# Kernel optimization log

Measured on AMD Instinct MI355X. Metric: run time of the kernel, lower is better.

## Reference

```python
import jax, jax.numpy as jnp
import numpy as np

N, E, DIN, EIN, H, R, G, DEPTH = 50000, 800000, 64, 16, 300, 1024, 256, 5


def setup_inputs() -> dict:
    key = jax.random.key(0)
    ks = jax.random.split(key, 16)
    x = jax.random.normal(ks[0], (N, DIN), jnp.float32)
    edge_attr = jax.random.normal(ks[1], (E, EIN), jnp.float32)
    edge_index = jax.random.randint(ks[2], (2, E), 0, N, dtype=jnp.int32)
    batch = jnp.sort(jax.random.randint(ks[3], (N,), 0, G, dtype=jnp.int32))
    def lin(k, fan_in, shape):
        return jax.random.normal(k, shape, jnp.float32) / np.sqrt(fan_in)
    return {
        "x": x,
        "edge_attr": edge_attr,
        "edge_index": edge_index,
        "batch": batch,
        "W_pn": lin(ks[4], DIN, (DIN, H)),
        "b_pn": jnp.zeros((H,), jnp.float32),
        "W_pe": lin(ks[5], EIN, (EIN, H)),
        "b_pe": jnp.zeros((H,), jnp.float32),
        "W1": lin(ks[6], H, (DEPTH, H, H)),
        "b1": jnp.zeros((DEPTH, H), jnp.float32),
        "W2": lin(ks[7], H, (DEPTH, H, H)),
        "b2": jnp.zeros((DEPTH, H), jnp.float32),
        "W_sp": lin(ks[8], H, (H, R)),
        "b_sp": jnp.zeros((R,), jnp.float32),
        "prelu_a": jnp.float32(0.25),
    }


def reference(x, edge_attr, edge_index, batch, W_pn, b_pn, W_pe, b_pe,
              W1, b1, W2, b2, W_sp, b_sp, prelu_a):
    src = edge_index[0]  # message source (x_j)
    dst = edge_index[1]  # aggregation target
    # input projections
    h = jax.nn.relu(x @ W_pn + b_pn)          # [N, H]
    e = edge_attr @ W_pe + b_pe               # [E, H]
    for i in range(DEPTH):
        # GINEConv: sum_j ReLU(x_j + e_ji), eps = 0
        m = jax.nn.relu(h[src] + e)            # [E, H]
        agg = jax.ops.segment_sum(m, dst, num_segments=N)  # [N, H]
        z = h + agg
        z = jax.nn.relu(z @ W1[i] + b1[i]) @ W2[i] + b2[i]
        h = jax.nn.relu(z) if i < DEPTH - 1 else z
        # dropout is identity in eval mode
    pooled = jax.ops.segment_sum(h, batch, num_segments=G)  # [G, H]
    out = pooled @ W_sp + b_sp                 # [G, R]
    # PReLU with a single learned slope
    return jnp.where(out >= 0, out, prelu_a * out)
```

## Files before the change

### kernel.cpp

```cpp
#include <hip/hip_runtime.h>
#include <hip/hip_bf16.h>

#define N_NODES 50000
#define N_EDGES 800000
#define DIN_    64
#define EIN_    16
#define H_      300
#define R_OUT   1024
#define G_GR    256
#define DEPTH_  5
#define KPAD    320
#define NPAD    50048
#define ESLOT   20

typedef unsigned short ushort_t;
typedef __attribute__((ext_vector_type(8))) short bf16x8;
typedef __attribute__((ext_vector_type(4))) short s16x4;
typedef __attribute__((ext_vector_type(4))) float f32x4;

__device__ __forceinline__ ushort_t f2b(float f) {
  unsigned x = __float_as_uint(f);
  unsigned r = (x + 0x7fffu + ((x >> 16) & 1u)) >> 16;
  return (ushort_t)r;
}
__device__ __forceinline__ float b2f(ushort_t u) {
  return __uint_as_float((unsigned)u << 16);
}

__global__ void pack_weights(const float* __restrict__ W1, const float* __restrict__ W2,
                             ushort_t* __restrict__ Bp1, ushort_t* __restrict__ Bp2) {
  int idx = blockIdx.x * 256 + threadIdx.x;
  const int per = DEPTH_ * 40 * KPAD * 8;
  if (idx >= 2 * per) return;
  const float* W = W1;
  ushort_t* Bp = Bp1;
  int t = idx;
  if (t >= per) { t -= per; W = W2; Bp = Bp2; }
  int j  = t & 7;
  int n  = (t >> 3) % KPAD;
  int kg = ((t >> 3) / KPAD) % 40;
  int i  = t / (40 * KPAD * 8);
  int k  = kg * 8 + j;
  float v = (k < H_ && n < H_) ? W[(i * H_ + k) * H_ + n] : 0.f;
  Bp[t] = f2b(v);
}

__global__ void pack_wpe(const float* __restrict__ Wpe, const float* __restrict__ bpe,
                         ushort_t* __restrict__ Bpe) {
  int t = blockIdx.x * 256 + threadIdx.x;
  if (t >= 4 * KPAD * 8) return;
  int j  = t & 7;
  int n  = (t >> 3) % KPAD;
  int kg = (t >> 3) / KPAD;
  int k  = kg * 8 + j;
  float v = 0.f;
  if (n < H_) {
    if (k < EIN_) v = Wpe[k * H_ + n];
    else if (k == EIN_) v = bpe[n];
  }
  Bpe[t] = f2b(v);
}

__global__ void pack_wpn(const float* __restrict__ Wpn, ushort_t* __restrict__ Bpn) {
  int t = blockIdx.x * 256 + threadIdx.x;
  if (t >= 8 * KPAD * 8) return;
  int j  = t & 7;
  int n  = (t >> 3) % KPAD;
  int kg = (t >> 3) / KPAD;
  int k  = kg * 8 + j;
  float v = (n < H_) ? Wpn[k * H_ + n] : 0.f;
  Bpn[t] = f2b(v);
}

__global__ void hist_deg(const int* __restrict__ dst, int* __restrict__ deg) {
  int e = blockIdx.x * 256 + threadIdx.x;
  if (e < N_EDGES) atomicAdd(deg + dst[e], 1);
}

__global__ __launch_bounds__(1024) void exscan_kernel(const int* __restrict__ deg,
                                                      int* __restrict__ off) {
  __shared__ int wsum[16];
  __shared__ int carry_s;
  int lane = threadIdx.x & 63;
  int wv = threadIdx.x >> 6;
  if (threadIdx.x == 0) carry_s = 0;
  __syncthreads();
  for (int base = 0; base < N_NODES; base += 1024) {
    int i = base + (int)threadIdx.x;
    int orig = (i < N_NODES) ? deg[i] : 0;
    int v = orig;
#pragma unroll
    for (int s = 1; s < 64; s <<= 1) {
      int u = __shfl_up(v, s);
      if (lane >= s) v += u;
    }
    if (lane == 63) wsum[wv] = v;
    __syncthreads();
    if (wv == 0) {
      int t = (lane < 16) ? wsum[lane] : 0;
#pragma unroll
      for (int s = 1; s < 16; s <<= 1) {
        int u = __shfl_up(t, s);
        if (lane >= s) t += u;
      }
      if (lane < 16) wsum[lane] = t;
    }
    __syncthreads();
    int wbase = (wv > 0) ? wsum[wv - 1] : 0;
    if (i < N_NODES) off[i] = carry_s + wbase + v - orig;
    __syncthreads();
    if (threadIdx.x == 1023) carry_s += wsum[15];
    __syncthreads();
  }
  if (threadIdx.x == 0) off[N_NODES] = carry_s;
}

__global__ void scatter_edges(const int* __restrict__ src, const int* __restrict__ dst,
                              int* __restrict__ cursor, int* __restrict__ csr_src,
                              int* __restrict__ csr_eid) {
  int e = blockIdx.x * 256 + threadIdx.x;
  if (e >= N_EDGES) return;
  int d = dst[e];
  int pos = atomicAdd(cursor + d, 1);
  csr_src[pos] = src[e];
  csr_eid[pos] = e;
}

__global__ __launch_bounds__(256) void proj_gemm(const float* __restrict__ x,
                                                 const ushort_t* __restrict__ Bpn,
                                                 const float* __restrict__ bpn,
                                                 ushort_t* __restrict__ hb) {
  int lane = threadIdx.x & 63;
  int wid  = threadIdx.x >> 6;
  int lr = lane & 15, lg = lane >> 4;
  int rowblk  = blockIdx.x * 64 + (wid & 1) * 32;
  int colbase = (wid >> 1) * 160;
  int ar0 = rowblk + lr;       if (ar0 >= N_NODES) ar0 = 0;
  int ar1 = rowblk + 16 + lr;  if (ar1 >= N_NODES) ar1 = 0;
  f32x4 acc[2][10];
#pragma unroll
  for (int a = 0; a < 2; ++a)
#pragma unroll
    for (int c = 0; c < 10; ++c) acc[a][c] = (f32x4){0.f, 0.f, 0.f, 0.f};

#pragma unroll
  for (int ks = 0; ks < 2; ++ks) {
    int k0 = ks * 32;
    const float* xr0 = x + (size_t)ar0 * DIN_ + k0 + lg * 8;
    const float* xr1 = x + (size_t)ar1 * DIN_ + k0 + lg * 8;
    f32x4 l0 = *(const f32x4*)xr0, h0 = *(const f32x4*)(xr0 + 4);
    f32x4 l1 = *(const f32x4*)xr1, h1 = *(const f32x4*)(xr1 + 4);
    bf16x8 a0, a1;
#pragma unroll
    for (int j = 0; j < 4; ++j) {
      a0[j] = (short)f2b(l0[j]); a0[j + 4] = (short)f2b(h0[j]);
      a1[j] = (short)f2b(l1[j]); a1[j + 4] = (short)f2b(h1[j]);
    }
    const ushort_t* bb = Bpn + ((unsigned)(k0 / 8 + lg) * KPAD + colbase + lr) * 8;
#pragma unroll
    for (int c = 0; c < 10; ++c) {
      bf16x8 b = *(const bf16x8*)(bb + c * 16 * 8);
      acc[0][c] = __builtin_amdgcn_mfma_f32_16x16x32_bf16(a0, b, acc[0][c], 0, 0, 0);
      acc[1][c] = __builtin_amdgcn_mfma_f32_16x16x32_bf16(a1, b, acc[1][c], 0, 0, 0);
    }
  }
#pragma unroll
  for (int rt = 0; rt < 2; ++rt) {
#pragma unroll
    for (int c = 0; c < 10; ++c) {
      int col = colbase + c * 16 + lr;
      float bv = (col < H_) ? bpn[col] : 0.f;
#pragma unroll
      for (int r = 0; r < 4; ++r) {
        int row = rowblk + rt * 16 + lg * 4 + r;
        if (row >= N_NODES) continue;
        float v = fmaxf(acc[rt][c][r] + bv, 0.f);
        if (col >= H_) v = 0.f;
        hb[(unsigned)row * KPAD + col] = f2b(v);
      }
    }
  }
}

__global__ __launch_bounds__(320) void node_agg_mfma(const ushort_t* __restrict__ hb,
                                                     const float* __restrict__ ea,
                                                     const ushort_t* __restrict__ Bpe,
                                                     const int* __restrict__ csr_src,
                                                     const int* __restrict__ csr_eid,
                                                     const int* __restrict__ off,
                                                     ushort_t* zb) {
  __shared__ ushort_t lds_e[2 * KPAD * ESLOT];
  int n = blockIdx.x;
  int tid = threadIdx.x;
  if (n >= N_NODES) {
    zb[(unsigned)n * KPAD + tid] = 0;
    return;
  }
  int lane = tid & 63;
  int w = tid >> 6;
  int lr = lane & 15, lg = lane >> 4;
  int p0 = __builtin_amdgcn_readfirstlane(off[n]);
  int p1 = __builtin_amdgcn_readfirstlane(off[n + 1]);
  unsigned zi = (unsigned)n * KPAD + tid;
  float self = b2f(hb[zi]);

  bf16x8 bfr[4];
#pragma unroll
  for (int t = 0; t < 4; ++t) {
    int col = w * 64 + t * 16 + lr;
    bfr[t] = *(const bf16x8*)(Bpe + ((unsigned)lg * KPAD + col) * 8);
  }

  float acc = 0.f;
  int ci = 0;
  for (int pc = p0; pc < p1; pc += 16, ci ^= 1) {
    int eid = csr_eid[pc + lr];
    bf16x8 afr = (bf16x8){0, 0, 0, 0, 0, 0, 0, 0};
    if (lg < 2) {
      const float* ar = ea + (size_t)eid * EIN_ + lg * 8;
      f32x4 lo = *(const f32x4*)ar;
      f32x4 hi = *(const f32x4*)(ar + 4);
#pragma unroll
      for (int j = 0; j < 4; ++j) {
        afr[j] = (short)f2b(lo[j]);
        afr[j + 4] = (short)f2b(hi[j]);
      }
    } else if (lg == 2) {
      afr[0] = (short)0x3F80;
    }
    int ebase = lg * 4;
    ushort_t* ldsb = lds_e + ci * (KPAD * ESLOT);
#pragma unroll
    for (int t = 0; t < 4; ++t) {
      f32x4 e4 = __builtin_amdgcn_mfma_f32_16x16x32_bf16(afr, bfr[t], (f32x4){0.f, 0.f, 0.f, 0.f}, 0, 0, 0);
      int col = w * 64 + t * 16 + lr;
      s16x4 pk;
#pragma unroll
      for (int r = 0; r < 4; ++r)
        pk[r] = (short)((pc + ebase + r < p1) ? f2b(e4[r]) : (ushort_t)0xFF80);
      *(s16x4*)(ldsb + (unsigned)col * ESLOT + ebase) = pk;
    }
    int sv = csr_src[pc + lr];
    __syncthreads();
    const ushort_t* ldsr = lds_e + ci * (KPAD * ESLOT) + (unsigned)tid * ESLOT;
#pragma unroll
    for (int eq = 0; eq < 4; ++eq) {
      if (pc + eq * 4 >= p1) break;
      s16x4 ep = *(const s16x4*)(ldsr + eq * 4);
#pragma unroll
      for (int r = 0; r < 4; ++r) {
        int s = __builtin_amdgcn_readlane(sv, eq * 4 + r);
        float g = b2f(hb[(unsigned)s * KPAD + tid]);
        acc += fmaxf(g + b2f((ushort_t)ep[r]), 0.f);
      }
    }
  }
  zb[zi] = f2b(self + acc);
}

template <int RELU_OUT, int OUT_BF16>
__global__ __launch_bounds__(256) void gemm300(const ushort_t* A,
                                               const ushort_t* __restrict__ Bp,
                                               const float* __restrict__ bias,
                                               void* Cout) {
  int lane = threadIdx.x & 63;
  int wid  = threadIdx.x >> 6;
  int lr = lane & 15, lg = lane >> 4;
  int rowblk  = blockIdx.x * 128 + (wid & 1) * 64;
  int colbase = (wid >> 1) * 160;
  f32x4 acc[4][10];
#pragma unroll
  for (int a = 0; a < 4; ++a)
#pragma unroll
    for (int c = 0; c < 10; ++c) acc[a][c] = (f32x4){0.f, 0.f, 0.f, 0.f};

  const ushort_t* Ap = A + (unsigned)(rowblk + lr) * KPAD + lg * 8;
  for (int k0 = 0; k0 < KPAD; k0 += 32) {
    bf16x8 a0 = *(const bf16x8*)(Ap + k0);
    bf16x8 a1 = *(const bf16x8*)(Ap + 16 * KPAD + k0);
    bf16x8 a2 = *(const bf16x8*)(Ap + 32 * KPAD + k0);
    bf16x8 a3 = *(const bf16x8*)(Ap + 48 * KPAD + k0);
    const ushort_t* bb = Bp + ((unsigned)(k0 / 8 + lg) * KPAD + colbase + lr) * 8;
#pragma unroll
    for (int c = 0; c < 10; ++c) {
      bf16x8 b = *(const bf16x8*)(bb + c * 16 * 8);
      acc[0][c] = __builtin_amdgcn_mfma_f32_16x16x32_bf16(a0, b, acc[0][c], 0, 0, 0);
      acc[1][c] = __builtin_amdgcn_mfma_f32_16x16x32_bf16(a1, b, acc[1][c], 0, 0, 0);
      acc[2][c] = __builtin_amdgcn_mfma_f32_16x16x32_bf16(a2, b, acc[2][c], 0, 0, 0);
      acc[3][c] = __builtin_amdgcn_mfma_f32_16x16x32_bf16(a3, b, acc[3][c], 0, 0, 0);
    }
  }
  __syncthreads();
#pragma unroll
  for (int rt = 0; rt < 4; ++rt) {
#pragma unroll
    for (int c = 0; c < 10; ++c) {
      int col = colbase + c * 16 + lr;
      float bv = (col < H_) ? bias[col] : 0.f;
#pragma unroll
      for (int r = 0; r < 4; ++r) {
        int row = rowblk + rt * 16 + lg * 4 + r;
        if (row >= N_NODES) continue;
        float v = acc[rt][c][r] + bv;
        if (RELU_OUT) v = fmaxf(v, 0.f);
        if (OUT_BF16) {
          ((ushort_t*)Cout)[(unsigned)row * KPAD + col] = f2b(v);
        } else if (col < H_) {
          ((float*)Cout)[(unsigned)row * H_ + col] = v;
        }
      }
    }
  }
}

__global__ void pool_kernel(const float* __restrict__ h, const int* __restrict__ batch,
                            float* __restrict__ pooled) {
  int g = blockIdx.x;
  int hh = threadIdx.x;
  int lo = 0, hi = N_NODES;
  while (lo < hi) { int mid = (lo + hi) >> 1; if (batch[mid] < g) lo = mid + 1; else hi = mid; }
  int start = lo;
  hi = N_NODES;
  while (lo < hi) { int mid = (lo + hi) >> 1; if (batch[mid] < g + 1) lo = mid + 1; else hi = mid; }
  int end = lo;
  if (hh >= H_) return;
  float s = 0.f;
  for (int n = start; n < end; ++n) s += h[(unsigned)n * H_ + hh];
  pooled[g * H_ + hh] = s;
}

__global__ void final_kernel(const float* __restrict__ pooled, const float* __restrict__ Wsp,
                             const float* __restrict__ bsp, const float* __restrict__ pa,
                             float* __restrict__ out) {
  int f = blockIdx.x * 256 + threadIdx.x;
  if (f >= G_GR * R_OUT) return;
  int g = f >> 10, r = f & 1023;
  float acc = bsp[r];
  const float* pr = pooled + g * H_;
  const float* wc = Wsp + r;
  for (int k = 0; k < H_; ++k) acc += pr[k] * wc[k * R_OUT];
  float a = pa[0];
  out[f] = acc >= 0.f ? acc : a * acc;
}

extern "C" void kernel_launch(void* const* d_in, const int* in_sizes, int n_in,
                              void* d_out, int out_size, void* d_ws, size_t ws_size,
                              hipStream_t stream) {
  const float* x   = (const float*)d_in[0];
  const float* ea  = (const float*)d_in[1];
  const int*   ei  = (const int*)d_in[2];
  const int*   bat = (const int*)d_in[3];
  const float* Wpn = (const float*)d_in[4];
  const float* bpn = (const float*)d_in[5];
  const float* Wpe = (const float*)d_in[6];
  const float* bpe = (const float*)d_in[7];
  const float* W1  = (const float*)d_in[8];
  const float* b1  = (const float*)d_in[9];
  const float* W2  = (const float*)d_in[10];
  const float* b2  = (const float*)d_in[11];
  const float* Wsp = (const float*)d_in[12];
  const float* bsp = (const float*)d_in[13];
  const float* pa  = (const float*)d_in[14];
  const int* src = ei;
  const int* dst = ei + N_EDGES;

  char* ws = (char*)d_ws;
  size_t off_b = 0;
  auto alloc = [&](size_t bytes) {
    void* p = ws + off_b;
    off_b += (bytes + 255) & ~(size_t)255;
    return p;
  };
  ushort_t* hb      = (ushort_t*)alloc(sizeof(ushort_t) * (size_t)NPAD * KPAD);
  ushort_t* zb      = (ushort_t*)alloc(sizeof(ushort_t) * (size_t)NPAD * KPAD);
  float*    h       = (float*)alloc(sizeof(float) * (size_t)N_NODES * H_);
  ushort_t* Bp1     = (ushort_t*)alloc(sizeof(ushort_t) * (size_t)DEPTH_ * 40 * KPAD * 8);
  ushort_t* Bp2     = (ushort_t*)alloc(sizeof(ushort_t) * (size_t)DEPTH_ * 40 * KPAD * 8);
  ushort_t* Bpe     = (ushort_t*)alloc(sizeof(ushort_t) * (size_t)4 * KPAD * 8);
  ushort_t* Bpn     = (ushort_t*)alloc(sizeof(ushort_t) * (size_t)8 * KPAD * 8);
  float*    pooled  = (float*)alloc(sizeof(float) * (size_t)G_GR * H_);
  int*      deg     = (int*)alloc(sizeof(int) * N_NODES);
  int*      offs    = (int*)alloc(sizeof(int) * (N_NODES + 1));
  int*      cursor  = (int*)alloc(sizeof(int) * N_NODES);
  int*      csr_src = (int*)alloc(sizeof(int) * (N_EDGES + 16));
  int*      csr_eid = (int*)alloc(sizeof(int) * (N_EDGES + 16));

  hipMemsetAsync(deg, 0, sizeof(int) * N_NODES, stream);
  hipMemsetAsync(csr_src + N_EDGES, 0, 16 * sizeof(int), stream);
  hipMemsetAsync(csr_eid + N_EDGES, 0, 16 * sizeof(int), stream);
  hist_deg<<<(N_EDGES + 255) / 256, 256, 0, stream>>>(dst, deg);
  exscan_kernel<<<1, 1024, 0, stream>>>(deg, offs);
  hipMemcpyAsync(cursor, offs, sizeof(int) * N_NODES, hipMemcpyDeviceToDevice, stream);
  scatter_edges<<<(N_EDGES + 255) / 256, 256, 0, stream>>>(src, dst, cursor, csr_src, csr_eid);

  pack_weights<<<(2 * DEPTH_ * 40 * KPAD * 8 + 255) / 256, 256, 0, stream>>>(W1, W2, Bp1, Bp2);
  pack_wpe<<<(4 * KPAD * 8 + 255) / 256, 256, 0, stream>>>(Wpe, bpe, Bpe);
  pack_wpn<<<(8 * KPAD * 8 + 255) / 256, 256, 0, stream>>>(Wpn, Bpn);
  proj_gemm<<<NPAD / 64, 256, 0, stream>>>(x, Bpn, bpn, hb);

  for (int i = 0; i < DEPTH_; ++i) {
    node_agg_mfma<<<NPAD, 320, 0, stream>>>(hb, ea, Bpe, csr_src, csr_eid, offs, zb);
    gemm300<1, 1><<<NPAD / 128, 256, 0, stream>>>(zb, Bp1 + (size_t)i * 40 * KPAD * 8, b1 + i * H_, zb);
    if (i < DEPTH_ - 1)
      gemm300<1, 1><<<NPAD / 128, 256, 0, stream>>>(zb, Bp2 + (size_t)i * 40 * KPAD * 8, b2 + i * H_, hb);
    else
      gemm300<0, 0><<<NPAD / 128, 256, 0, stream>>>(zb, Bp2 + (size_t)i * 40 * KPAD * 8, b2 + i * H_, h);
  }

  pool_kernel<<<G_GR, 320, 0, stream>>>(h, bat, pooled);
  final_kernel<<<(G_GR * R_OUT) / 256, 256, 0, stream>>>(pooled, Wsp, bsp, pa, (float*)d_out);
}
```

Baseline: 2.089 ms.

## Use packed bf16 converts, halve GEMM row tile, and split graph pooling

Replaces the scalar round-to-nearest float-to-bf16 conversions in the projection and edge-aggregation kernels with the v_cvt_pk_bf16_f32 packed instruction. The edge-validity predicates are hoisted out of the MFMA loop. The node GEMM now gives each block 64 rows instead of 128, doubling the grid to fill the GPU better and cutting accumulator registers. Pooling is split into four partial sums per graph plus a combine kernel to add parallelism, at the cost of an extra launch and scratch buffer.

```diff
diff --git a/kernel.cpp b/kernel.cpp
--- a/kernel.cpp
+++ b/kernel.cpp
@@ -1,5 +1,6 @@
 #include <hip/hip_runtime.h>
 #include <hip/hip_bf16.h>
+#include <math.h>
 
 #define N_NODES 50000
 #define N_EDGES 800000
@@ -25,6 +26,11 @@
 }
 __device__ __forceinline__ float b2f(ushort_t u) {
   return __uint_as_float((unsigned)u << 16);
+}
+__device__ __forceinline__ unsigned cvtpk(float lo, float hi) {
+  unsigned r;
+  asm("v_cvt_pk_bf16_f32 %0, %1, %2" : "=v"(r) : "v"(lo), "v"(hi));
+  return r;
 }
 
 __global__ void pack_weights(const float* __restrict__ W1, const float* __restrict__ W2,
@@ -150,18 +156,17 @@
     const float* xr1 = x + (size_t)ar1 * DIN_ + k0 + lg * 8;
     f32x4 l0 = *(const f32x4*)xr0, h0 = *(const f32x4*)(xr0 + 4);
     f32x4 l1 = *(const f32x4*)xr1, h1 = *(const f32x4*)(xr1 + 4);
-    bf16x8 a0, a1;
-#pragma unroll
-    for (int j = 0; j < 4; ++j) {
-      a0[j] = (short)f2b(l0[j]); a0[j + 4] = (short)f2b(h0[j]);
-      a1[j] = (short)f2b(l1[j]); a1[j + 4] = (short)f2b(h1[j]);
-    }
+    union { bf16x8 v; unsigned u[4]; } a0, a1;
+    a0.u[0] = cvtpk(l0[0], l0[1]); a0.u[1] = cvtpk(l0[2], l0[3]);
+    a0.u[2] = cvtpk(h0[0], h0[1]); a0.u[3] = cvtpk(h0[2], h0[3]);
+    a1.u[0] = cvtpk(l1[0], l1[1]); a1.u[1] = cvtpk(l1[2], l1[3]);
+    a1.u[2] = cvtpk(h1[0], h1[1]); a1.u[3] = cvtpk(h1[2], h1[3]);
     const ushort_t* bb = Bpn + ((unsigned)(k0 / 8 + lg) * KPAD + colbase + lr) * 8;
 #pragma unroll
     for (int c = 0; c < 10; ++c) {
       bf16x8 b = *(const bf16x8*)(bb + c * 16 * 8);
-      acc[0][c] = __builtin_amdgcn_mfma_f32_16x16x32_bf16(a0, b, acc[0][c], 0, 0, 0);
-      acc[1][c] = __builtin_amdgcn_mfma_f32_16x16x32_bf16(a1, b, acc[1][c], 0, 0, 0);
+      acc[0][c] = __builtin_amdgcn_mfma_f32_16x16x32_bf16(a0.v, b, acc[0][c], 0, 0, 0);
+      acc[1][c] = __builtin_amdgcn_mfma_f32_16x16x32_bf16(a1.v, b, acc[1][c], 0, 0, 0);
     }
   }
 #pragma unroll
@@ -215,30 +220,33 @@
   int ci = 0;
   for (int pc = p0; pc < p1; pc += 16, ci ^= 1) {
     int eid = csr_eid[pc + lr];
-    bf16x8 afr = (bf16x8){0, 0, 0, 0, 0, 0, 0, 0};
+    union { bf16x8 v; unsigned u[4]; } afr;
+    afr.u[0] = afr.u[1] = afr.u[2] = afr.u[3] = 0u;
     if (lg < 2) {
       const float* ar = ea + (size_t)eid * EIN_ + lg * 8;
       f32x4 lo = *(const f32x4*)ar;
       f32x4 hi = *(const f32x4*)(ar + 4);
-#pragma unroll
-      for (int j = 0; j < 4; ++j) {
-        afr[j] = (short)f2b(lo[j]);
-        afr[j + 4] = (short)f2b(hi[j]);
-      }
+      afr.u[0] = cvtpk(lo[0], lo[1]); afr.u[1] = cvtpk(lo[2], lo[3]);
+      afr.u[2] = cvtpk(hi[0], hi[1]); afr.u[3] = cvtpk(hi[2], hi[3]);
     } else if (lg == 2) {
-      afr[0] = (short)0x3F80;
+      afr.u[0] = 0x3F80u;
     }
     int ebase = lg * 4;
+    bool v0 = (pc + ebase + 0 < p1), v1 = (pc + ebase + 1 < p1);
+    bool v2 = (pc + ebase + 2 < p1), v3 = (pc + ebase + 3 < p1);
     ushort_t* ldsb = lds_e + ci * (KPAD * ESLOT);
 #pragma unroll
     for (int t = 0; t < 4; ++t) {
-      f32x4 e4 = __builtin_amdgcn_mfma_f32_16x16x32_bf16(afr, bfr[t], (f32x4){0.f, 0.f, 0.f, 0.f}, 0, 0, 0);
+      f32x4 e4 = __builtin_amdgcn_mfma_f32_16x16x32_bf16(afr.v, bfr[t], (f32x4){0.f, 0.f, 0.f, 0.f}, 0, 0, 0);
       int col = w * 64 + t * 16 + lr;
-      s16x4 pk;
-#pragma unroll
-      for (int r = 0; r < 4; ++r)
-        pk[r] = (short)((pc + ebase + r < p1) ? f2b(e4[r]) : (ushort_t)0xFF80);
-      *(s16x4*)(ldsb + (unsigned)col * ESLOT + ebase) = pk;
+      float f0 = v0 ? e4[0] : -INFINITY;
+      float f1 = v1 ? e4[1] : -INFINITY;
+      float f2 = v2 ? e4[2] : -INFINITY;
+      float f3 = v3 ? e4[3] : -INFINITY;
+      union { s16x4 v; unsigned u[2]; } pk;
+      pk.u[0] = cvtpk(f0, f1);
+      pk.u[1] = cvtpk(f2, f3);
+      *(s16x4*)(ldsb + (unsigned)col * ESLOT + ebase) = pk.v;
     }
     int sv = csr_src[pc + lr];
     __syncthreads();
@@ -266,11 +274,11 @@
   int lane = threadIdx.x & 63;
   int wid  = threadIdx.x >> 6;
   int lr = lane & 15, lg = lane >> 4;
-  int rowblk  = blockIdx.x * 128 + (wid & 1) * 64;
+  int rowblk  = blockIdx.x * 64 + (wid & 1) * 32;
   int colbase = (wid >> 1) * 160;
-  f32x4 acc[4][10];
-#pragma unroll
-  for (int a = 0; a < 4; ++a)
+  f32x4 acc[2][10];
+#pragma unroll
+  for (int a = 0; a < 2; ++a)
 #pragma unroll
     for (int c = 0; c < 10; ++c) acc[a][c] = (f32x4){0.f, 0.f, 0.f, 0.f};
 
@@ -278,21 +286,17 @@
   for (int k0 = 0; k0 < KPAD; k0 += 32) {
     bf16x8 a0 = *(const bf16x8*)(Ap + k0);
     bf16x8 a1 = *(const bf16x8*)(Ap + 16 * KPAD + k0);
-    bf16x8 a2 = *(const bf16x8*)(Ap + 32 * KPAD + k0);
-    bf16x8 a3 = *(const bf16x8*)(Ap + 48 * KPAD + k0);
     const ushort_t* bb = Bp + ((unsigned)(k0 / 8 + lg) * KPAD + colbase + lr) * 8;
 #pragma unroll
     for (int c = 0; c < 10; ++c) {
       bf16x8 b = *(const bf16x8*)(bb + c * 16 * 8);
       acc[0][c] = __builtin_amdgcn_mfma_f32_16x16x32_bf16(a0, b, acc[0][c], 0, 0, 0);
       acc[1][c] = __builtin_amdgcn_mfma_f32_16x16x32_bf16(a1, b, acc[1][c], 0, 0, 0);
-      acc[2][c] = __builtin_amdgcn_mfma_f32_16x16x32_bf16(a2, b, acc[2][c], 0, 0, 0);
-      acc[3][c] = __builtin_amdgcn_mfma_f32_16x16x32_bf16(a3, b, acc[3][c], 0, 0, 0);
     }
   }
   __syncthreads();
 #pragma unroll
-  for (int rt = 0; rt < 4; ++rt) {
+  for (int rt = 0; rt < 2; ++rt) {
 #pragma unroll
     for (int c = 0; c < 10; ++c) {
       int col = colbase + c * 16 + lr;
@@ -314,8 +318,9 @@
 }
 
 __global__ void pool_kernel(const float* __restrict__ h, const int* __restrict__ batch,
-                            float* __restrict__ pooled) {
-  int g = blockIdx.x;
+                            float* __restrict__ pooled4) {
+  int g = blockIdx.x >> 2;
+  int q = blockIdx.x & 3;
   int hh = threadIdx.x;
   int lo = 0, hi = N_NODES;
   while (lo < hi) { int mid = (lo + hi) >> 1; if (batch[mid] < g) lo = mid + 1; else hi = mid; }
@@ -324,9 +329,20 @@
   while (lo < hi) { int mid = (lo + hi) >> 1; if (batch[mid] < g + 1) lo = mid + 1; else hi = mid; }
   int end = lo;
   if (hh >= H_) return;
-  float s = 0.f;
-  for (int n = start; n < end; ++n) s += h[(unsigned)n * H_ + hh];
-  pooled[g * H_ + hh] = s;
+  int len = end - start;
+  int chunk = (len + 3) >> 2;
+  int s = start + q * chunk;
+  int e = s + chunk; if (e > end) e = end;
+  float sum = 0.f;
+  for (int n = s; n < e; ++n) sum += h[(unsigned)n * H_ + hh];
+  pooled4[((unsigned)q * G_GR + g) * H_ + hh] = sum;
+}
+
+__global__ void pool_combine(const float* __restrict__ pooled4, float* __restrict__ pooled) {
+  int f = blockIdx.x * 256 + threadIdx.x;
+  if (f >= G_GR * H_) return;
+  float s = pooled4[f] + pooled4[G_GR * H_ + f] + pooled4[2 * G_GR * H_ + f] + pooled4[3 * G_GR * H_ + f];
+  pooled[f] = s;
 }
 
 __global__ void final_kernel(const float* __restrict__ pooled, const float* __restrict__ Wsp,
@@ -379,6 +395,7 @@
   ushort_t* Bpe     = (ushort_t*)alloc(sizeof(ushort_t) * (size_t)4 * KPAD * 8);
   ushort_t* Bpn     = (ushort_t*)alloc(sizeof(ushort_t) * (size_t)8 * KPAD * 8);
   float*    pooled  = (float*)alloc(sizeof(float) * (size_t)G_GR * H_);
+  float*    pooled4 = (float*)alloc(sizeof(float) * (size_t)4 * G_GR * H_);
   int*      deg     = (int*)alloc(sizeof(int) * N_NODES);
   int*      offs    = (int*)alloc(sizeof(int) * (N_NODES + 1));
   int*      cursor  = (int*)alloc(sizeof(int) * N_NODES);
@@ -400,13 +417,14 @@
 
   for (int i = 0; i < DEPTH_; ++i) {
     node_agg_mfma<<<NPAD, 320, 0, stream>>>(hb, ea, Bpe, csr_src, csr_eid, offs, zb);
-    gemm300<1, 1><<<NPAD / 128, 256, 0, stream>>>(zb, Bp1 + (size_t)i * 40 * KPAD * 8, b1 + i * H_, zb);
+    gemm300<1, 1><<<NPAD / 64, 256, 0, stream>>>(zb, Bp1 + (size_t)i * 40 * KPAD * 8, b1 + i * H_, zb);
     if (i < DEPTH_ - 1)
-      gemm300<1, 1><<<NPAD / 128, 256, 0, stream>>>(zb, Bp2 + (size_t)i * 40 * KPAD * 8, b2 + i * H_, hb);
+      gemm300<1, 1><<<NPAD / 64, 256, 0, stream>>>(zb, Bp2 + (size_t)i * 40 * KPAD * 8, b2 + i * H_, hb);
     else
-      gemm300<0, 0><<<NPAD / 128, 256, 0, stream>>>(zb, Bp2 + (size_t)i * 40 * KPAD * 8, b2 + i * H_, h);
-  }
-
-  pool_kernel<<<G_GR, 320, 0, stream>>>(h, bat, pooled);
+      gemm300<0, 0><<<NPAD / 64, 256, 0, stream>>>(zb, Bp2 + (size_t)i * 40 * KPAD * 8, b2 + i * H_, h);
+  }
+
+  pool_kernel<<<G_GR * 4, 320, 0, stream>>>(h, bat, pooled4);
+  pool_combine<<<(G_GR * H_ + 255) / 256, 256, 0, stream>>>(pooled4, pooled);
   final_kernel<<<(G_GR * R_OUT) / 256, 256, 0, stream>>>(pooled, Wsp, bsp, pa, (float*)d_out);
 }
```

Result: faster. 1.793 ms (-14.2%).
